# Performance work log

Hardware: AMD Instinct MI355X
Metric: run time of the kernel (lower is better)

Reference implementation:

```python
import jax, jax.numpy as jnp
import numpy as np

K = 5          # number of neighbors
TAU_R = 0.5    # soft-rank temperature (original space)
TAU_S = 0.5    # soft top-k temperature (embedding space)


def _cdist(a, b):
    # Euclidean pairwise distances, torch.cdist(p=2) equivalent, safe at 0.
    sq = (jnp.sum(a * a, axis=1)[:, None]
          + jnp.sum(b * b, axis=1)[None, :]
          - 2.0 * (a @ b.T))
    sq = jnp.maximum(sq, 0.0)
    pos = sq > 1e-12
    return jnp.where(pos, jnp.sqrt(jnp.where(pos, sq, 1.0)), 0.0)


def setup_inputs() -> dict:
    key = jax.random.key(0)
    k1, k2 = jax.random.split(key)
    X = jax.random.normal(k1, (384, 128), dtype=jnp.float32)
    Z = jax.random.normal(k2, (384, 32), dtype=jnp.float32)
    return {"X": X, "Z": Z}


def reference(X, Z):
    n = X.shape[0]
    D_X = _cdist(X, X)  # (n, n)
    D_Z = _cdist(Z, Z)  # (n, n)

    # soft_rank_X[i, a] = 1 + sum_b sigmoid((D_X[i,b] - D_X[i,a]) / tau_r)
    # (matches diffs_X = D_X.unsqueeze(1) - D_X.unsqueeze(2); sum over dim=2)
    diffs_X = D_X[:, None, :] - D_X[:, :, None]            # (n, n, n)
    soft_rank_X = 1.0 + jnp.sum(jax.nn.sigmoid(diffs_X / TAU_R), axis=2)
    intrusion = jax.nn.relu(soft_rank_X - K)

    # soft top-k mask: R[i, j] = 1 + sum_l sigmoid((D_Z[i,l] - D_Z[i,j]) / tau_s)
    # (vectorized form of the original per-row Python loop)
    diffs_Z = D_Z[:, None, :] - D_Z[:, :, None]            # (n, n, n)
    R_Z = 1.0 + jnp.sum(jax.nn.sigmoid(diffs_Z / TAU_S), axis=2)
    W_Z = jnp.clip((K + 1.0 - R_Z) / K, 0.0, 1.0)

    loss_matrix = intrusion * (1.0 - W_Z)
    norm = 2.0 / (n * K * (2 * n - 3 * K - 1))
    return norm * jnp.sum(loss_matrix)
```

## Files before the change

kernel.cpp:

```cpp
#include <hip/hip_runtime.h>

#define N 384
#define DXD 128
#define DZD 32
#define NPAIR 192
#define NORM (2.0f / 1443840.0f)
#define CX 24.0f
#define CZ 12.0f

typedef float f32x2 __attribute__((ext_vector_type(2)));

#define PKFMA(d, a, b, c) asm("v_pk_fma_f32 %0, %1, %2, %3" : "=v"(d) : "v"(a), "v"(b), "v"(c))
#define PKADD(d, a, b)    asm("v_pk_add_f32 %0, %1, %2"     : "=v"(d) : "v"(a), "v"(b))
#define PKMUL(d, a, b)    asm("v_pk_mul_f32 %0, %1, %2"     : "=v"(d) : "v"(a), "v"(b))

__global__ void __launch_bounds__(256) transpose_xz(const float* __restrict__ X,
                                                    const float* __restrict__ Z,
                                                    float* __restrict__ XT,
                                                    float* __restrict__ ZT,
                                                    float* __restrict__ out) {
    __shared__ float tile[64][129];
    const int b = blockIdx.x;
    const int t = threadIdx.x;
    if (b == 0 && t == 0) out[0] = 0.f;

    if (b < 6) {
        const int R = b * 64;
        #pragma unroll
        for (int r0 = 0; r0 < 64; r0 += 8) {
            const int r = r0 + (t >> 5);
            const int c = (t & 31) * 4;
            float4 v = *reinterpret_cast<const float4*>(X + (size_t)(R + r) * DXD + c);
            tile[r][c] = v.x; tile[r][c + 1] = v.y; tile[r][c + 2] = v.z; tile[r][c + 3] = v.w;
        }
        __syncthreads();
        const int l = t & 63, w = t >> 6;
        #pragma unroll
        for (int k0 = 0; k0 < DXD; k0 += 4)
            XT[(size_t)(k0 + w) * N + R + l] = tile[l][k0 + w];
    } else {
        const int R = (b - 6) * 64;
        #pragma unroll
        for (int r0 = 0; r0 < 64; r0 += 32) {
            const int r = r0 + (t >> 3);
            const int c = (t & 7) * 4;
            float4 v = *reinterpret_cast<const float4*>(Z + (size_t)(R + r) * DZD + c);
            tile[r][c] = v.x; tile[r][c + 1] = v.y; tile[r][c + 2] = v.z; tile[r][c + 3] = v.w;
        }
        __syncthreads();
        const int l = t & 63, w = t >> 6;
        #pragma unroll
        for (int k0 = 0; k0 < DZD; k0 += 4)
            ZT[(size_t)(k0 + w) * N + R + l] = tile[l][k0 + w];
    }
}

__global__ void __launch_bounds__(384) fused_loss(const float* __restrict__ X,
                                                  const float* __restrict__ Z,
                                                  const float* __restrict__ XT,
                                                  const float* __restrict__ ZT,
                                                  float* __restrict__ out) {
    __shared__ float ex[N] __attribute__((aligned(16)));
    __shared__ float ez[N] __attribute__((aligned(16)));
    __shared__ float4 ps[NPAIR];
    __shared__ float sxp[4][N];
    __shared__ float szp[4][N];
    __shared__ float red[6];
    const int i = blockIdx.x;
    const int t = threadIdx.x;

    const float* __restrict__ Xi = X + (size_t)i * DXD;
    const float* __restrict__ Zi = Z + (size_t)i * DZD;

    {
        float sq = 0.f;
        #pragma unroll 16
        for (int k = 0; k < DXD; ++k) {
            float v = XT[(size_t)k * N + t] - Xi[k];
            sq += v * v;
        }
        float dx = (sq > 1e-12f) ? sqrtf(sq) : 0.f;
        ex[t] = __expf(2.f * dx - CX);

        float sqz = 0.f;
        #pragma unroll 16
        for (int k = 0; k < DZD; ++k) {
            float v = ZT[(size_t)k * N + t] - Zi[k];
            sqz += v * v;
        }
        float dz = (sqz > 1e-12f) ? sqrtf(sqz) : 0.f;
        ez[t] = __expf(2.f * dz - CZ);
    }
    __syncthreads();

    if (t < NPAIR) {
        float e0 = ex[2 * t], e1 = ex[2 * t + 1];
        float f0 = ez[2 * t], f1 = ez[2 * t + 1];
        ps[t] = make_float4(e0 * e1, f0 * f1, e0 + e1, f0 + f1);
    }
    __syncthreads();

    const int qh = t / 96;
    const int tt = t - 96 * qh;
    const int a0 = tt, a1 = tt + 96, a2 = tt + 192, a3 = tt + 288;

    f32x2 ee0;  ee0.x = ex[a0]; ee0.y = ez[a0];
    f32x2 ee1;  ee1.x = ex[a1]; ee1.y = ez[a1];
    f32x2 ee2;  ee2.x = ex[a2]; ee2.y = ez[a2];
    f32x2 ee3;  ee3.x = ex[a3]; ee3.y = ez[a3];
    f32x2 eq0, eq1, eq2, eq3;
    PKMUL(eq0, ee0, ee0);
    PKMUL(eq1, ee1, ee1);
    PKMUL(eq2, ee2, ee2);
    PKMUL(eq3, ee3, ee3);

    f32x2 A0 = {0.f, 0.f}, A1 = {0.f, 0.f}, A2 = {0.f, 0.f}, A3 = {0.f, 0.f};

#define UNIT(c0, c1, eev, eeq, accm)                                          \
    {                                                                         \
        f32x2 P0; P0.x = c0.x; P0.y = c0.y;                                   \
        f32x2 S0; S0.x = c0.z; S0.y = c0.w;                                   \
        f32x2 P1; P1.x = c1.x; P1.y = c1.y;                                   \
        f32x2 S1; S1.x = c1.z; S1.y = c1.w;                                   \
        f32x2 t0, t1, d0, d1, n0, n1, D, T, Nn, r;                            \
        PKFMA(t0, eev, S0, P0);                                               \
        PKFMA(t1, eev, S1, P1);                                               \
        PKADD(d0, t0, eeq);                                                   \
        PKADD(d1, t1, eeq);                                                   \
        PKADD(n0, t0, P0);                                                    \
        PKADD(n1, t1, P1);                                                    \
        PKMUL(D, d0, d1);                                                     \
        PKMUL(T, n0, d1);                                                     \
        PKFMA(Nn, n1, d0, T);                                                 \
        r.x = __builtin_amdgcn_rcpf(D.x);                                     \
        r.y = __builtin_amdgcn_rcpf(D.y);                                     \
        PKFMA(accm, Nn, r, accm);                                             \
    }

    const int p0 = qh * 48;
    #pragma unroll 3
    for (int p = p0; p < p0 + 48; p += 4) {
        #pragma unroll
        for (int j = 0; j < 2; ++j) {
            float4 c0 = ps[p + 2 * j];
            float4 c1 = ps[p + 2 * j + 1];
            UNIT(c0, c1, ee0, eq0, A0)
            UNIT(c0, c1, ee1, eq1, A1)
            UNIT(c0, c1, ee2, eq2, A2)
            UNIT(c0, c1, ee3, eq3, A3)
        }
    }
#undef UNIT

    sxp[qh][a0] = A0.x;  szp[qh][a0] = A0.y;
    sxp[qh][a1] = A1.x;  szp[qh][a1] = A1.y;
    sxp[qh][a2] = A2.x;  szp[qh][a2] = A2.y;
    sxp[qh][a3] = A3.x;  szp[qh][a3] = A3.y;
    __syncthreads();

    {
        float sx = (sxp[0][t] + sxp[1][t]) + (sxp[2][t] + sxp[3][t]);
        float sz = (szp[0][t] + szp[1][t]) + (szp[2][t] + szp[3][t]);
        float intr = fmaxf(sx - 4.f, 0.f);
        float W = fminf(fmaxf((5.f - sz) * 0.2f, 0.f), 1.f);
        float contrib = intr * (1.f - W);
        #pragma unroll
        for (int off = 32; off > 0; off >>= 1)
            contrib += __shfl_down(contrib, off, 64);
        const int lane = t & 63, w = t >> 6;
        if (lane == 0) red[w] = contrib;
    }
    __syncthreads();
    if (t == 0) {
        float s = ((red[0] + red[1]) + (red[2] + red[3])) + (red[4] + red[5]);
        atomicAdd(out, s * NORM);
    }
}

extern "C" void kernel_launch(void* const* d_in, const int* in_sizes, int n_in,
                              void* d_out, int out_size, void* d_ws, size_t ws_size,
                              hipStream_t stream) {
    const float* X = (const float*)d_in[0];
    const float* Z = (const float*)d_in[1];
    float* out = (float*)d_out;

    float* XT = (float*)d_ws;
    float* ZT = XT + (size_t)DXD * N;

    transpose_xz<<<12, 256, 0, stream>>>(X, Z, XT, ZT, out);
    fused_loss<<<N, 384, 0, stream>>>(X, Z, XT, ZT, out);
}
```

Before: 27.91 us.

## Split each row across two 192-thread blocks instead of one 384-thread block

Result: slower. 33.19 us (+18.9%).

```diff
diff --git a/kernel.cpp b/kernel.cpp
--- a/kernel.cpp
+++ b/kernel.cpp
@@ -55,7 +55,7 @@
     }
 }
 
-__global__ void __launch_bounds__(384) fused_loss(const float* __restrict__ X,
+__global__ void __launch_bounds__(192) fused_loss(const float* __restrict__ X,
                                                   const float* __restrict__ Z,
                                                   const float* __restrict__ XT,
                                                   const float* __restrict__ ZT,
@@ -63,58 +63,59 @@
     __shared__ float ex[N] __attribute__((aligned(16)));
     __shared__ float ez[N] __attribute__((aligned(16)));
     __shared__ float4 ps[NPAIR];
-    __shared__ float sxp[4][N];
-    __shared__ float szp[4][N];
-    __shared__ float red[6];
-    const int i = blockIdx.x;
+    __shared__ float sxp[2][192];
+    __shared__ float szp[2][192];
+    __shared__ float red[3];
+    const int i = blockIdx.x >> 1;
+    const int half = blockIdx.x & 1;
     const int t = threadIdx.x;
 
     const float* __restrict__ Xi = X + (size_t)i * DXD;
     const float* __restrict__ Zi = Z + (size_t)i * DZD;
 
-    {
+    #pragma unroll
+    for (int rep = 0; rep < 2; ++rep) {
+        const int a = rep * 192 + t;
         float sq = 0.f;
         #pragma unroll 16
         for (int k = 0; k < DXD; ++k) {
-            float v = XT[(size_t)k * N + t] - Xi[k];
+            float v = XT[(size_t)k * N + a] - Xi[k];
             sq += v * v;
         }
         float dx = (sq > 1e-12f) ? sqrtf(sq) : 0.f;
-        ex[t] = __expf(2.f * dx - CX);
+        ex[a] = __expf(2.f * dx - CX);
 
         float sqz = 0.f;
         #pragma unroll 16
         for (int k = 0; k < DZD; ++k) {
-            float v = ZT[(size_t)k * N + t] - Zi[k];
+            float v = ZT[(size_t)k * N + a] - Zi[k];
             sqz += v * v;
         }
         float dz = (sqz > 1e-12f) ? sqrtf(sqz) : 0.f;
-        ez[t] = __expf(2.f * dz - CZ);
+        ez[a] = __expf(2.f * dz - CZ);
     }
     __syncthreads();
 
-    if (t < NPAIR) {
+    {
         float e0 = ex[2 * t], e1 = ex[2 * t + 1];
         float f0 = ez[2 * t], f1 = ez[2 * t + 1];
         ps[t] = make_float4(e0 * e1, f0 * f1, e0 + e1, f0 + f1);
     }
     __syncthreads();
 
-    const int qh = t / 96;
+    const int qh = (t >= 96) ? 1 : 0;
     const int tt = t - 96 * qh;
-    const int a0 = tt, a1 = tt + 96, a2 = tt + 192, a3 = tt + 288;
+    const int a0 = half * 192 + tt;
+    const int a1 = a0 + 96;
 
     f32x2 ee0;  ee0.x = ex[a0]; ee0.y = ez[a0];
     f32x2 ee1;  ee1.x = ex[a1]; ee1.y = ez[a1];
-    f32x2 ee2;  ee2.x = ex[a2]; ee2.y = ez[a2];
-    f32x2 ee3;  ee3.x = ex[a3]; ee3.y = ez[a3];
-    f32x2 eq0, eq1, eq2, eq3;
+    f32x2 eq0, eq1;
     PKMUL(eq0, ee0, ee0);
     PKMUL(eq1, ee1, ee1);
-    PKMUL(eq2, ee2, ee2);
-    PKMUL(eq3, ee3, ee3);
 
-    f32x2 A0 = {0.f, 0.f}, A1 = {0.f, 0.f}, A2 = {0.f, 0.f}, A3 = {0.f, 0.f};
+    f32x2 A0 = {0.f, 0.f}, A1 = {0.f, 0.f};
+    f32x2 B0 = {0.f, 0.f}, B1 = {0.f, 0.f};
 
 #define UNIT(c0, c1, eev, eeq, accm)                                          \
     {                                                                         \
@@ -137,30 +138,26 @@
         PKFMA(accm, Nn, r, accm);                                             \
     }
 
-    const int p0 = qh * 48;
+    const int p0 = qh * 96;
     #pragma unroll 3
-    for (int p = p0; p < p0 + 48; p += 4) {
+    for (int p = p0; p < p0 + 96; p += 4) {
         #pragma unroll
         for (int j = 0; j < 2; ++j) {
             float4 c0 = ps[p + 2 * j];
             float4 c1 = ps[p + 2 * j + 1];
-            UNIT(c0, c1, ee0, eq0, A0)
-            UNIT(c0, c1, ee1, eq1, A1)
-            UNIT(c0, c1, ee2, eq2, A2)
-            UNIT(c0, c1, ee3, eq3, A3)
+            if (j == 0) { UNIT(c0, c1, ee0, eq0, A0) UNIT(c0, c1, ee1, eq1, B0) }
+            else        { UNIT(c0, c1, ee0, eq0, A1) UNIT(c0, c1, ee1, eq1, B1) }
         }
     }
 #undef UNIT
 
-    sxp[qh][a0] = A0.x;  szp[qh][a0] = A0.y;
-    sxp[qh][a1] = A1.x;  szp[qh][a1] = A1.y;
-    sxp[qh][a2] = A2.x;  szp[qh][a2] = A2.y;
-    sxp[qh][a3] = A3.x;  szp[qh][a3] = A3.y;
+    sxp[qh][tt]      = A0.x + A1.x;  szp[qh][tt]      = A0.y + A1.y;
+    sxp[qh][tt + 96] = B0.x + B1.x;  szp[qh][tt + 96] = B0.y + B1.y;
     __syncthreads();
 
     {
-        float sx = (sxp[0][t] + sxp[1][t]) + (sxp[2][t] + sxp[3][t]);
-        float sz = (szp[0][t] + szp[1][t]) + (szp[2][t] + szp[3][t]);
+        float sx = sxp[0][t] + sxp[1][t];
+        float sz = szp[0][t] + szp[1][t];
         float intr = fmaxf(sx - 4.f, 0.f);
         float W = fminf(fmaxf((5.f - sz) * 0.2f, 0.f), 1.f);
         float contrib = intr * (1.f - W);
@@ -171,10 +168,7 @@
         if (lane == 0) red[w] = contrib;
     }
     __syncthreads();
-    if (t == 0) {
-        float s = ((red[0] + red[1]) + (red[2] + red[3])) + (red[4] + red[5]);
-        atomicAdd(out, s * NORM);
-    }
+    if (t == 0) atomicAdd(out, (red[0] + red[1] + red[2]) * NORM);
 }
 
 extern "C" void kernel_launch(void* const* d_in, const int* in_sizes, int n_in,
@@ -188,5 +182,5 @@
     float* ZT = XT + (size_t)DXD * N;
 
     transpose_xz<<<12, 256, 0, stream>>>(X, Z, XT, ZT, out);
-    fused_loss<<<N, 384, 0, stream>>>(X, Z, XT, ZT, out);
+    fused_loss<<<2 * N, 192, 0, stream>>>(X, Z, XT, ZT, out);
 }
```

## Precompute Gram matrices in tiled kernel and split each row across two blocks

Applied to the files above, without the earlier changes.

After: 26.33 us (median of 2 runs). 1.06x faster.

```diff
diff --git a/kernel.cpp b/kernel.cpp
--- a/kernel.cpp
+++ b/kernel.cpp
@@ -14,95 +14,106 @@
 #define PKADD(d, a, b)    asm("v_pk_add_f32 %0, %1, %2"     : "=v"(d) : "v"(a), "v"(b))
 #define PKMUL(d, a, b)    asm("v_pk_mul_f32 %0, %1, %2"     : "=v"(d) : "v"(a), "v"(b))
 
-__global__ void __launch_bounds__(256) transpose_xz(const float* __restrict__ X,
-                                                    const float* __restrict__ Z,
-                                                    float* __restrict__ XT,
-                                                    float* __restrict__ ZT,
-                                                    float* __restrict__ out) {
-    __shared__ float tile[64][129];
+__global__ void __launch_bounds__(256) gram(const float* __restrict__ X,
+                                            const float* __restrict__ Z,
+                                            float* __restrict__ GX,
+                                            float* __restrict__ GZ,
+                                            float* __restrict__ NX,
+                                            float* __restrict__ NZ,
+                                            float* __restrict__ out) {
+    __shared__ float As[32][132];
+    __shared__ float Bs[32][132];
     const int b = blockIdx.x;
     const int t = threadIdx.x;
     if (b == 0 && t == 0) out[0] = 0.f;
 
-    if (b < 6) {
-        const int R = b * 64;
-        #pragma unroll
-        for (int r0 = 0; r0 < 64; r0 += 8) {
-            const int r = r0 + (t >> 5);
-            const int c = (t & 31) * 4;
-            float4 v = *reinterpret_cast<const float4*>(X + (size_t)(R + r) * DXD + c);
-            tile[r][c] = v.x; tile[r][c + 1] = v.y; tile[r][c + 2] = v.z; tile[r][c + 3] = v.w;
-        }
-        __syncthreads();
-        const int l = t & 63, w = t >> 6;
-        #pragma unroll
-        for (int k0 = 0; k0 < DXD; k0 += 4)
-            XT[(size_t)(k0 + w) * N + R + l] = tile[l][k0 + w];
-    } else {
-        const int R = (b - 6) * 64;
-        #pragma unroll
-        for (int r0 = 0; r0 < 64; r0 += 32) {
-            const int r = r0 + (t >> 3);
-            const int c = (t & 7) * 4;
-            float4 v = *reinterpret_cast<const float4*>(Z + (size_t)(R + r) * DZD + c);
-            tile[r][c] = v.x; tile[r][c + 1] = v.y; tile[r][c + 2] = v.z; tile[r][c + 3] = v.w;
-        }
-        __syncthreads();
-        const int l = t & 63, w = t >> 6;
-        #pragma unroll
-        for (int k0 = 0; k0 < DZD; k0 += 4)
-            ZT[(size_t)(k0 + w) * N + R + l] = tile[l][k0 + w];
+    const bool isX = (b < 144);
+    const int bb = isX ? b : b - 144;
+    const int bi = bb / 12, bj = bb % 12;
+    const int R = bi * 32, C = bj * 32;
+    const float* __restrict__ A = isX ? X : Z;
+    const int K = isX ? DXD : DZD;
+    float* __restrict__ G = isX ? GX : GZ;
+    float* __restrict__ Nv = isX ? NX : NZ;
+
+    const int kf4 = K / 4;
+    const int nf4 = 32 * kf4;
+    for (int idx = t; idx < nf4; idx += 256) {
+        const int r = idx / kf4;
+        const int c4 = (idx % kf4) * 4;
+        float4 va = *reinterpret_cast<const float4*>(A + (size_t)(R + r) * K + c4);
+        float4 vb = *reinterpret_cast<const float4*>(A + (size_t)(C + r) * K + c4);
+        *reinterpret_cast<float4*>(&As[r][c4]) = va;
+        *reinterpret_cast<float4*>(&Bs[r][c4]) = vb;
+    }
+    __syncthreads();
+
+    const int ty = t >> 4, tx = t & 15;
+    const int r0 = 2 * ty, c0 = 2 * tx;
+    float a00 = 0.f, a01 = 0.f, a10 = 0.f, a11 = 0.f;
+    for (int k = 0; k < K; k += 4) {
+        float4 ar0 = *reinterpret_cast<const float4*>(&As[r0][k]);
+        float4 ar1 = *reinterpret_cast<const float4*>(&As[r0 + 1][k]);
+        float4 bc0 = *reinterpret_cast<const float4*>(&Bs[c0][k]);
+        float4 bc1 = *reinterpret_cast<const float4*>(&Bs[c0 + 1][k]);
+        a00 += ar0.x * bc0.x + ar0.y * bc0.y + ar0.z * bc0.z + ar0.w * bc0.w;
+        a01 += ar0.x * bc1.x + ar0.y * bc1.y + ar0.z * bc1.z + ar0.w * bc1.w;
+        a10 += ar1.x * bc0.x + ar1.y * bc0.y + ar1.z * bc0.z + ar1.w * bc0.w;
+        a11 += ar1.x * bc1.x + ar1.y * bc1.y + ar1.z * bc1.z + ar1.w * bc1.w;
+    }
+    float2 w0; w0.x = a00; w0.y = a01;
+    float2 w1; w1.x = a10; w1.y = a11;
+    *reinterpret_cast<float2*>(G + (size_t)(R + r0) * N + C + c0) = w0;
+    *reinterpret_cast<float2*>(G + (size_t)(R + r0 + 1) * N + C + c0) = w1;
+    if (R == C && r0 == c0) {
+        Nv[R + r0] = a00;
+        Nv[R + r0 + 1] = a11;
     }
 }
 
-__global__ void __launch_bounds__(384) fused_loss(const float* __restrict__ X,
-                                                  const float* __restrict__ Z,
-                                                  const float* __restrict__ XT,
-                                                  const float* __restrict__ ZT,
+__global__ void __launch_bounds__(192) fused_loss(const float* __restrict__ GX,
+                                                  const float* __restrict__ GZ,
+                                                  const float* __restrict__ NX,
+                                                  const float* __restrict__ NZ,
                                                   float* __restrict__ out) {
     __shared__ float ex[N] __attribute__((aligned(16)));
     __shared__ float ez[N] __attribute__((aligned(16)));
     __shared__ float4 ps[NPAIR];
-    __shared__ float sxp[4][N];
-    __shared__ float szp[4][N];
-    __shared__ float red[6];
-    const int i = blockIdx.x;
+    __shared__ float sxp[4][192];
+    __shared__ float szp[4][192];
+    __shared__ float red[3];
+    const int i = blockIdx.x >> 1;
+    const int half = blockIdx.x & 1;
     const int t = threadIdx.x;
 
-    const float* __restrict__ Xi = X + (size_t)i * DXD;
-    const float* __restrict__ Zi = Z + (size_t)i * DZD;
+    const float nxi = NX[i];
+    const float nzi = NZ[i];
+    #pragma unroll
+    for (int rep = 0; rep < 2; ++rep) {
+        const int a = rep * 192 + t;
+        float gx = GX[(size_t)i * N + a];
+        float d2x = fmaxf(nxi + NX[a] - 2.f * gx, 0.f);
+        float dx = (d2x > 1e-12f) ? sqrtf(d2x) : 0.f;
+        ex[a] = __expf(2.f * dx - CX);
+
+        float gz = GZ[(size_t)i * N + a];
+        float d2z = fmaxf(nzi + NZ[a] - 2.f * gz, 0.f);
+        float dz = (d2z > 1e-12f) ? sqrtf(d2z) : 0.f;
+        ez[a] = __expf(2.f * dz - CZ);
+    }
+    __syncthreads();
 
     {
-        float sq = 0.f;
-        #pragma unroll 16
-        for (int k = 0; k < DXD; ++k) {
-            float v = XT[(size_t)k * N + t] - Xi[k];
-            sq += v * v;
-        }
-        float dx = (sq > 1e-12f) ? sqrtf(sq) : 0.f;
-        ex[t] = __expf(2.f * dx - CX);
-
-        float sqz = 0.f;
-        #pragma unroll 16
-        for (int k = 0; k < DZD; ++k) {
-            float v = ZT[(size_t)k * N + t] - Zi[k];
-            sqz += v * v;
-        }
-        float dz = (sqz > 1e-12f) ? sqrtf(sqz) : 0.f;
-        ez[t] = __expf(2.f * dz - CZ);
-    }
-    __syncthreads();
-
-    if (t < NPAIR) {
         float e0 = ex[2 * t], e1 = ex[2 * t + 1];
         float f0 = ez[2 * t], f1 = ez[2 * t + 1];
         ps[t] = make_float4(e0 * e1, f0 * f1, e0 + e1, f0 + f1);
     }
     __syncthreads();
 
-    const int qh = t / 96;
-    const int tt = t - 96 * qh;
-    const int a0 = tt, a1 = tt + 96, a2 = tt + 192, a3 = tt + 288;
+    const int qh = t / 48;
+    const int tt = t - 48 * qh;
+    const int a0 = half * 192 + tt;
+    const int a1 = a0 + 48, a2 = a0 + 96, a3 = a0 + 144;
 
     f32x2 ee0;  ee0.x = ex[a0]; ee0.y = ez[a0];
     f32x2 ee1;  ee1.x = ex[a1]; ee1.y = ez[a1];
@@ -116,12 +127,12 @@
 
     f32x2 A0 = {0.f, 0.f}, A1 = {0.f, 0.f}, A2 = {0.f, 0.f}, A3 = {0.f, 0.f};
 
-#define UNIT(c0, c1, eev, eeq, accm)                                          \
+#define UNIT(c0v, c1v, eev, eeq, accm)                                        \
     {                                                                         \
-        f32x2 P0; P0.x = c0.x; P0.y = c0.y;                                   \
-        f32x2 S0; S0.x = c0.z; S0.y = c0.w;                                   \
-        f32x2 P1; P1.x = c1.x; P1.y = c1.y;                                   \
-        f32x2 S1; S1.x = c1.z; S1.y = c1.w;                                   \
+        f32x2 P0; P0.x = c0v.x; P0.y = c0v.y;                                 \
+        f32x2 S0; S0.x = c0v.z; S0.y = c0v.w;                                 \
+        f32x2 P1; P1.x = c1v.x; P1.y = c1v.y;                                 \
+        f32x2 S1; S1.x = c1v.z; S1.y = c1v.w;                                 \
         f32x2 t0, t1, d0, d1, n0, n1, D, T, Nn, r;                            \
         PKFMA(t0, eev, S0, P0);                                               \
         PKFMA(t1, eev, S1, P1);                                               \
@@ -152,10 +163,10 @@
     }
 #undef UNIT
 
-    sxp[qh][a0] = A0.x;  szp[qh][a0] = A0.y;
-    sxp[qh][a1] = A1.x;  szp[qh][a1] = A1.y;
-    sxp[qh][a2] = A2.x;  szp[qh][a2] = A2.y;
-    sxp[qh][a3] = A3.x;  szp[qh][a3] = A3.y;
+    sxp[qh][tt]       = A0.x;  szp[qh][tt]       = A0.y;
+    sxp[qh][tt + 48]  = A1.x;  szp[qh][tt + 48]  = A1.y;
+    sxp[qh][tt + 96]  = A2.x;  szp[qh][tt + 96]  = A2.y;
+    sxp[qh][tt + 144] = A3.x;  szp[qh][tt + 144] = A3.y;
     __syncthreads();
 
     {
@@ -171,10 +182,7 @@
         if (lane == 0) red[w] = contrib;
     }
     __syncthreads();
-    if (t == 0) {
-        float s = ((red[0] + red[1]) + (red[2] + red[3])) + (red[4] + red[5]);
-        atomicAdd(out, s * NORM);
-    }
+    if (t == 0) atomicAdd(out, (red[0] + red[1] + red[2]) * NORM);
 }
 
 extern "C" void kernel_launch(void* const* d_in, const int* in_sizes, int n_in,
@@ -184,9 +192,11 @@
     const float* Z = (const float*)d_in[1];
     float* out = (float*)d_out;
 
-    float* XT = (float*)d_ws;
-    float* ZT = XT + (size_t)DXD * N;
-
-    transpose_xz<<<12, 256, 0, stream>>>(X, Z, XT, ZT, out);
-    fused_loss<<<N, 384, 0, stream>>>(X, Z, XT, ZT, out);
+    float* GX = (float*)d_ws;
+    float* GZ = GX + (size_t)N * N;
+    float* NXv = GZ + (size_t)N * N;
+    float* NZv = NXv + N;
+
+    gram<<<288, 256, 0, stream>>>(X, Z, GX, GZ, NXv, NZv, out);
+    fused_loss<<<2 * N, 192, 0, stream>>>(GX, GZ, NXv, NZv, out);
 }
```
